# Kernel optimization log

Measured on AMD Instinct MI355X. Metric: run time of the kernel, lower is better.

## Reference

```python
import jax, jax.numpy as jnp
import numpy as np

DIM = 256
HEADS = 8
DIM_HEAD = 64
INNER = HEADS * DIM_HEAD  # 512
SCALE = DIM_HEAD ** -0.5
EPS = 1e-5


def _layernorm(x, w, b):
    mu = jnp.mean(x, axis=-1, keepdims=True)
    var = jnp.var(x, axis=-1, keepdims=True)
    return (x - mu) * jax.lax.rsqrt(var + EPS) * w + b


def setup_inputs() -> dict:
    key = jax.random.key(0)
    ks = jax.random.split(key, 20)
    B, N, M, H, W = 8, 4096, 256, 64, 64
    s = 0.02
    inp = {
        "feat": jax.random.normal(ks[0], (B, N, DIM), jnp.float32),
        "center": jax.random.normal(ks[1], (B, M, DIM), jnp.float32),
        "pos": jax.random.normal(ks[2], (B, DIM, H, W), jnp.float32),
        "center_pos": jax.random.normal(ks[3], (B, M, DIM), jnp.float32),
        # projection weights stored [in, out] so y = x @ W
        "Wq": jax.random.normal(ks[4], (DIM, INNER), jnp.float32) * s,
        "Wk": jax.random.normal(ks[5], (DIM, INNER), jnp.float32) * s,
        "Wv1": jax.random.normal(ks[6], (DIM, INNER), jnp.float32) * s,
        "Wv2": jax.random.normal(ks[7], (DIM, INNER), jnp.float32) * s,
        "Wo1": jax.random.normal(ks[8], (INNER, DIM), jnp.float32) * s,
        "Wo2": jax.random.normal(ks[9], (INNER, DIM), jnp.float32) * s,
        "ln1_w": jnp.ones((DIM,), jnp.float32),
        "ln1_b": jnp.zeros((DIM,), jnp.float32),
        "ln2_w": jnp.ones((DIM,), jnp.float32),
        "ln2_b": jnp.zeros((DIM,), jnp.float32),
        "ffn1_W1": jax.random.normal(ks[10], (DIM, DIM), jnp.float32) * s,
        "ffn1_W2": jax.random.normal(ks[11], (DIM, DIM), jnp.float32) * s,
        "ffn1_b2": jnp.zeros((DIM,), jnp.float32),
        "ffn2_W1": jax.random.normal(ks[12], (DIM, DIM), jnp.float32) * s,
        "ffn2_W2": jax.random.normal(ks[13], (DIM, DIM), jnp.float32) * s,
        "ffn2_b2": jnp.zeros((DIM,), jnp.float32),
    }
    return inp


def reference(feat, center, pos, center_pos, Wq, Wk, Wv1, Wv2, Wo1, Wo2,
              ln1_w, ln1_b, ln2_w, ln2_b, ffn1_W1, ffn1_W2, ffn1_b2,
              ffn2_W1, ffn2_W2, ffn2_b2):
    B = feat.shape[0]
    # pos: [B, C, H, W] -> [B, N, C]
    pos_f = pos.reshape(B, DIM, -1).transpose(0, 2, 1)
    q = (feat + pos_f) @ Wq            # [B, N, INNER]
    k = (center + center_pos) @ Wk     # [B, M, INNER]
    v1 = feat @ Wv1                    # [B, N, INNER]
    v2 = center @ Wv2                  # [B, M, INNER]

    def split(x):  # [B, T, h*d] -> [B, h, T, d]
        return x.reshape(B, x.shape[1], HEADS, DIM_HEAD).transpose(0, 2, 1, 3)

    q, k, v1, v2 = split(q), split(k), split(v1), split(v2)
    attn = jnp.einsum("bhnd,bhmd->bhnm", q, k) * SCALE  # [B, h, N, M]
    attn1 = jax.nn.softmax(attn, axis=-2)  # over N (queries)
    attn2 = jax.nn.softmax(attn, axis=-1)  # over M (keys)
    out_feat = jnp.einsum("bhnm,bhmd->bhnd", attn2, v2)    # [B, h, N, d]
    out_center = jnp.einsum("bhnm,bhnd->bhmd", attn1, v1)  # [B, h, M, d]

    def merge(x):  # [B, h, T, d] -> [B, T, h*d]
        return x.transpose(0, 2, 1, 3).reshape(B, x.shape[2], INNER)

    out_feat = merge(out_feat) @ Wo1 + feat
    out_center = merge(out_center) @ Wo2 + center
    out_feat = _layernorm(out_feat, ln1_w, ln1_b)
    out_center = _layernorm(out_center, ln2_w, ln2_b)
    out_feat = jax.nn.relu(out_feat @ ffn1_W1) @ ffn1_W2 + ffn1_b2 + out_feat
    out_center = jax.nn.relu(out_center @ ffn2_W1) @ ffn2_W2 + ffn2_b2 + out_center
    return out_feat, out_center
```

## Files before the change

### kernel.cpp

```cpp
#include <hip/hip_runtime.h>

typedef __bf16 bf16;
typedef __bf16 bf16x4 __attribute__((ext_vector_type(4)));
typedef __bf16 bf16x8 __attribute__((ext_vector_type(8)));
typedef float f32x4 __attribute__((ext_vector_type(4)));

#define MFMA16(a, b, c) __builtin_amdgcn_mfma_f32_16x16x32_bf16(a, b, c, 0, 0, 0)

#define CEXP 0.18033688011112042f

struct WTArgs {
  const float* src[10];
  bf16* dst[10];
  int K[10];
  int N[10];
};

__global__ __launch_bounds__(256) void wtrans_kernel(WTArgs args) {
  const int z = blockIdx.z;
  const int K = args.K[z], N = args.N[z];
  const int k0 = blockIdx.x * 64, n0 = blockIdx.y * 64;
  if (k0 >= K || n0 >= N) return;
  __shared__ float t[64][65];
  const int tx = threadIdx.x & 63, ty = threadIdx.x >> 6;
  const float* __restrict__ src = args.src[z];
  bf16* __restrict__ dst = args.dst[z];
#pragma unroll
  for (int i = 0; i < 16; ++i)
    t[ty + i * 4][tx] = src[(size_t)(k0 + ty + i * 4) * N + n0 + tx];
  __syncthreads();
#pragma unroll
  for (int i = 0; i < 16; ++i)
    dst[(size_t)(n0 + ty + i * 4) * K + k0 + tx] = (bf16)t[tx][ty + i * 4];
}

__global__ __launch_bounds__(256) void prep_xq_kernel(
    const float* __restrict__ feat, const float* __restrict__ pos,
    bf16* __restrict__ xq) {
  const int n0 = blockIdx.x * 64;
  const int c0 = blockIdx.y * 64;
  const int b = blockIdx.z;
  __shared__ float t[64][65];
  const int tx = threadIdx.x & 63, ty = threadIdx.x >> 6;
#pragma unroll
  for (int i = 0; i < 16; ++i) {
    int c = ty + i * 4;
    t[c][tx] = pos[((size_t)b * 256 + c0 + c) * 4096 + n0 + tx];
  }
  __syncthreads();
#pragma unroll
  for (int i = 0; i < 16; ++i) {
    int n = ty + i * 4;
    size_t off = ((size_t)b * 4096 + n0 + n) * 256 + c0 + tx;
    xq[off] = (bf16)(feat[off] + t[tx][n]);
  }
}

__global__ __launch_bounds__(256) void addvec_kernel(
    const float* __restrict__ a, const float* __restrict__ b,
    bf16* __restrict__ o, int n4) {
  int i = blockIdx.x * 256 + threadIdx.x;
  if (i < n4) {
    f32x4 x = ((const f32x4*)a)[i];
    f32x4 y = ((const f32x4*)b)[i];
    bf16x4 z;
#pragma unroll
    for (int j = 0; j < 4; ++j) z[j] = (bf16)(x[j] + y[j]);
    ((bf16x4*)o)[i] = z;
  }
}

template <typename TA>
__device__ inline bf16x8 ldA8(const TA* p);
template <>
__device__ inline bf16x8 ldA8<bf16>(const bf16* p) {
  return *(const bf16x8*)p;
}
template <>
__device__ inline bf16x8 ldA8<float>(const float* p) {
  f32x4 u = *(const f32x4*)p;
  f32x4 v = *((const f32x4*)p + 1);
  bf16x8 o;
#pragma unroll
  for (int i = 0; i < 4; ++i) {
    o[i] = (bf16)u[i];
    o[4 + i] = (bf16)v[i];
  }
  return o;
}

template <int EPI, typename TO, typename TR, typename TA>
__global__ __launch_bounds__(256) void gemm_kernel(
    const TA* __restrict__ A, const bf16* __restrict__ BT,
    TO* __restrict__ C, const TR* __restrict__ resid,
    const float* __restrict__ bias, int M, int N, int K) {
  const int m0 = blockIdx.x * 128;
  const int n0 = blockIdx.y * 128;
  const int tid = threadIdx.x;
  const int lane = tid & 63;
  const int w = tid >> 6;
  const int wr = (w >> 1) * 64, wc = (w & 1) * 64;
  const int l15 = lane & 15, quad = lane >> 4;

  __shared__ bf16 Al[128 * 40];
  __shared__ bf16 Bl[128 * 40];

  f32x4 acc[4][4];
#pragma unroll
  for (int i = 0; i < 4; ++i)
#pragma unroll
    for (int j = 0; j < 4; ++j) acc[i][j] = (f32x4){0.f, 0.f, 0.f, 0.f};

  for (int k0 = 0; k0 < K; k0 += 32) {
#pragma unroll
    for (int c = 0; c < 2; ++c) {
      int idx = tid + c * 256;
      int row = idx >> 2;
      int ko = (idx & 3) * 8;
      *(bf16x8*)(Al + row * 40 + ko) =
          ldA8(A + (size_t)(m0 + row) * K + k0 + ko);
      *(bf16x8*)(Bl + row * 40 + ko) =
          *(const bf16x8*)(BT + (size_t)(n0 + row) * K + k0 + ko);
    }
    __syncthreads();
    bf16x8 fa[4], fb[4];
#pragma unroll
    for (int i = 0; i < 4; ++i) {
      fa[i] = *(const bf16x8*)(Al + (wr + i * 16 + l15) * 40 + quad * 8);
      fb[i] = *(const bf16x8*)(Bl + (wc + i * 16 + l15) * 40 + quad * 8);
    }
#pragma unroll
    for (int i = 0; i < 4; ++i)
#pragma unroll
      for (int j = 0; j < 4; ++j)
        acc[i][j] = MFMA16(fa[i], fb[j], acc[i][j]);
    __syncthreads();
  }

#pragma unroll
  for (int i = 0; i < 4; ++i) {
#pragma unroll
    for (int r = 0; r < 4; ++r) {
      int row = m0 + wr + i * 16 + quad * 4 + r;
      size_t rb = (size_t)row * N + n0 + wc;
#pragma unroll
      for (int j = 0; j < 4; ++j) {
        int col = j * 16 + l15;
        float v = acc[i][j][r];
        if constexpr (EPI == 1) v = fmaxf(v, 0.f);
        if constexpr (EPI == 2) v += (float)resid[rb + col];
        if constexpr (EPI == 3)
          v += bias[n0 + wc + col] + (float)resid[rb + col];
        C[rb + col] = (TO)v;
      }
    }
  }
}

__global__ __launch_bounds__(256) void attf_kernel(
    const bf16* q, const bf16* __restrict__ kk, const bf16* __restrict__ v1,
    const bf16* __restrict__ v2, bf16* af, float* __restrict__ acc_c,
    float* __restrict__ colsum) {
  const int nb = blockIdx.x;
  const int h = blockIdx.y;
  const int b = blockIdx.z;
  const int tid = threadIdx.x;
  const int lane = tid & 63;
  const int w = tid >> 6;
  const int l15 = lane & 15, quad = lane >> 4;

  __shared__ bf16 klds[64 * 72];
  __shared__ bf16 v2T[64 * 72];
  __shared__ bf16 v1T[64 * 72];
  __shared__ bf16 PT[64 * 72];
  __shared__ bf16 Pl[4][16 * 72];

  f32x4 oc2[16];
#pragma unroll
  for (int i = 0; i < 16; ++i) oc2[i] = (f32x4){0.f, 0.f, 0.f, 0.f};
  float cs[16];
#pragma unroll
  for (int i = 0; i < 16; ++i) cs[i] = 0.f;

  for (int ch = 0; ch < 8; ++ch) {
    int nrow = b * 4096 + nb * 512 + ch * 64 + w * 16 + l15;
    const bf16* qp = q + (size_t)nrow * 512 + h * 64 + quad * 8;
    bf16x8 a0 = *(const bf16x8*)(qp);
    bf16x8 a1 = *(const bf16x8*)(qp + 32);

    f32x4 o1[4];
#pragma unroll
    for (int i = 0; i < 4; ++i) o1[i] = (f32x4){0.f, 0.f, 0.f, 0.f};
    float rs[4] = {0.f, 0.f, 0.f, 0.f};

    for (int mq = 0; mq < 4; ++mq) {
      __syncthreads();
#pragma unroll
      for (int c = 0; c < 2; ++c) {
        int idx = tid + c * 256;
        int m = idx >> 3, dc = (idx & 7) * 8;
        *(bf16x8*)(klds + m * 72 + dc) = *(const bf16x8*)(
            kk + ((size_t)(b * 256 + mq * 64 + m)) * 512 + h * 64 + dc);
      }
#pragma unroll
      for (int c = 0; c < 16; ++c) {
        int idx = tid + c * 256;
        int m = idx >> 6, d = idx & 63;
        v2T[d * 72 + m] =
            v2[((size_t)(b * 256 + mq * 64 + m)) * 512 + h * 64 + d];
      }
      if (mq == 0) {
#pragma unroll
        for (int c = 0; c < 16; ++c) {
          int idx = tid + c * 256;
          int nl = idx >> 6, d = idx & 63;
          v1T[d * 72 + nl] = v1[((size_t)(b * 4096 + nb * 512 + ch * 64 + nl)) *
                                    512 + h * 64 + d];
        }
      }
      __syncthreads();

#pragma unroll
      for (int mt = 0; mt < 4; ++mt) {
        const bf16* kp = klds + (mt * 16 + l15) * 72 + quad * 8;
        bf16x8 b0 = *(const bf16x8*)(kp);
        bf16x8 b1 = *(const bf16x8*)(kp + 32);
        f32x4 s = (f32x4){0.f, 0.f, 0.f, 0.f};
        s = MFMA16(a0, b0, s);
        s = MFMA16(a1, b1, s);
        float e0 = exp2f(s[0] * CEXP);
        float e1 = exp2f(s[1] * CEXP);
        float e2 = exp2f(s[2] * CEXP);
        float e3 = exp2f(s[3] * CEXP);
        rs[0] += e0; rs[1] += e1; rs[2] += e2; rs[3] += e3;
        cs[mq * 4 + mt] += e0 + e1 + e2 + e3;
        Pl[w][(quad * 4 + 0) * 72 + mt * 16 + l15] = (bf16)e0;
        Pl[w][(quad * 4 + 1) * 72 + mt * 16 + l15] = (bf16)e1;
        Pl[w][(quad * 4 + 2) * 72 + mt * 16 + l15] = (bf16)e2;
        Pl[w][(quad * 4 + 3) * 72 + mt * 16 + l15] = (bf16)e3;
        bf16x4 ev;
        ev[0] = (bf16)e0; ev[1] = (bf16)e1; ev[2] = (bf16)e2; ev[3] = (bf16)e3;
        *(bf16x4*)(PT + (mt * 16 + l15) * 72 + w * 16 + quad * 4) = ev;
      }
      __syncthreads();

#pragma unroll
      for (int ks = 0; ks < 2; ++ks) {
        bf16x8 pa = *(const bf16x8*)(Pl[w] + l15 * 72 + ks * 32 + quad * 8);
#pragma unroll
        for (int dt = 0; dt < 4; ++dt) {
          bf16x8 vb =
              *(const bf16x8*)(v2T + (dt * 16 + l15) * 72 + ks * 32 + quad * 8);
          o1[dt] = MFMA16(pa, vb, o1[dt]);
        }
      }
#pragma unroll
      for (int ks = 0; ks < 2; ++ks) {
        bf16x8 pa2 =
            *(const bf16x8*)(PT + (w * 16 + l15) * 72 + ks * 32 + quad * 8);
#pragma unroll
        for (int dt = 0; dt < 4; ++dt) {
          bf16x8 vb =
              *(const bf16x8*)(v1T + (dt * 16 + l15) * 72 + ks * 32 + quad * 8);
          oc2[mq * 4 + dt] = MFMA16(pa2, vb, oc2[mq * 4 + dt]);
        }
      }
    }

    float inv[4];
#pragma unroll
    for (int r = 0; r < 4; ++r) {
      float v = rs[r];
      v += __shfl_xor(v, 1, 64);
      v += __shfl_xor(v, 2, 64);
      v += __shfl_xor(v, 4, 64);
      v += __shfl_xor(v, 8, 64);
      inv[r] = 1.f / v;
    }
#pragma unroll
    for (int dt = 0; dt < 4; ++dt) {
#pragma unroll
      for (int r = 0; r < 4; ++r) {
        int n = nb * 512 + ch * 64 + w * 16 + quad * 4 + r;
        af[((size_t)(b * 4096 + n)) * 512 + h * 64 + dt * 16 + l15] =
            (bf16)(o1[dt][r] * inv[r]);
      }
    }
  }

#pragma unroll
  for (int t = 0; t < 16; ++t) {
    float v = cs[t];
    v += __shfl_xor(v, 16, 64);
    v += __shfl_xor(v, 32, 64);
    if (quad == 0)
      atomicAdd(&colsum[(b * 8 + h) * 256 + (t >> 2) * 64 + (t & 3) * 16 + l15],
                v);
  }
  float* base = acc_c + ((size_t)(b * 8 + h)) * 256 * 64;
#pragma unroll
  for (int mq = 0; mq < 4; ++mq) {
#pragma unroll
    for (int dt = 0; dt < 4; ++dt) {
#pragma unroll
      for (int r = 0; r < 4; ++r) {
        int m = mq * 64 + w * 16 + quad * 4 + r;
        atomicAdd(base + m * 64 + dt * 16 + l15, oc2[mq * 4 + dt][r]);
      }
    }
  }
}

__global__ __launch_bounds__(256) void acm_kernel(
    const float* __restrict__ acc_c, const float* __restrict__ colsum,
    bf16* __restrict__ acm) {
  int idx = blockIdx.x * 256 + threadIdx.x;
  int d = idx & 63;
  int h = (idx >> 6) & 7;
  int m = (idx >> 9) & 255;
  int b = idx >> 17;
  float cv = colsum[(b * 8 + h) * 256 + m];
  float v = acc_c[(((size_t)(b * 8 + h)) * 256 + m) * 64 + d] / cv;
  acm[idx] = (bf16)v;
}

__global__ __launch_bounds__(256) void ln_kernel(
    const bf16* __restrict__ x, const float* __restrict__ wv,
    const float* __restrict__ bv, bf16* __restrict__ y, int rows) {
  int wave = threadIdx.x >> 6;
  int lane = threadIdx.x & 63;
  int row = blockIdx.x * 4 + wave;
  if (row >= rows) return;
  const bf16* xr = x + (size_t)row * 256;
  bf16x4 v = *(const bf16x4*)(xr + lane * 4);
  float f0 = v[0], f1 = v[1], f2 = v[2], f3 = v[3];
  float s = f0 + f1 + f2 + f3;
  float ss = f0 * f0 + f1 * f1 + f2 * f2 + f3 * f3;
#pragma unroll
  for (int m = 1; m < 64; m <<= 1) {
    s += __shfl_xor(s, m, 64);
    ss += __shfl_xor(ss, m, 64);
  }
  float mean = s * (1.f / 256.f);
  float var = ss * (1.f / 256.f) - mean * mean;
  float rstd = rsqrtf(var + 1e-5f);
  f32x4 wq = *(const f32x4*)(wv + lane * 4);
  f32x4 bq = *(const f32x4*)(bv + lane * 4);
  bf16x4 o;
  o[0] = (bf16)((f0 - mean) * rstd * wq[0] + bq[0]);
  o[1] = (bf16)((f1 - mean) * rstd * wq[1] + bq[1]);
  o[2] = (bf16)((f2 - mean) * rstd * wq[2] + bq[2]);
  o[3] = (bf16)((f3 - mean) * rstd * wq[3] + bq[3]);
  *(bf16x4*)(y + (size_t)row * 256 + lane * 4) = o;
}

extern "C" void kernel_launch(void* const* d_in, const int* in_sizes, int n_in,
                              void* d_out, int out_size, void* d_ws,
                              size_t ws_size, hipStream_t stream) {
  const float* feat = (const float*)d_in[0];
  const float* center = (const float*)d_in[1];
  const float* pos = (const float*)d_in[2];
  const float* cpos = (const float*)d_in[3];
  const float* Wq = (const float*)d_in[4];
  const float* Wk = (const float*)d_in[5];
  const float* Wv1 = (const float*)d_in[6];
  const float* Wv2 = (const float*)d_in[7];
  const float* Wo1 = (const float*)d_in[8];
  const float* Wo2 = (const float*)d_in[9];
  const float* ln1w = (const float*)d_in[10];
  const float* ln1b = (const float*)d_in[11];
  const float* ln2w = (const float*)d_in[12];
  const float* ln2b = (const float*)d_in[13];
  const float* f1W1 = (const float*)d_in[14];
  const float* f1W2 = (const float*)d_in[15];
  const float* f1b2 = (const float*)d_in[16];
  const float* f2W1 = (const float*)d_in[17];
  const float* f2W2 = (const float*)d_in[18];
  const float* f2b2 = (const float*)d_in[19];

  char* ws = (char*)d_ws;
  const size_t MB = 1024 * 1024;
  bf16* q_ = (bf16*)(ws + 0);
  bf16* af_ = q_;
  bf16* v1_ = (bf16*)(ws + 32 * MB);
  bf16* xq_ = (bf16*)(ws + 64 * MB);
  bf16* rf_ = xq_;
  bf16* k_ = (bf16*)(ws + 80 * MB);
  bf16* xk_ = (bf16*)(ws + 82 * MB);
  bf16* rc_ = xk_;
  bf16* v2_ = (bf16*)(ws + 83 * MB);
  bf16* acm_ = v2_;
  float* acc_ = (float*)(ws + 85 * MB);
  float* colsum_ = (float*)(ws + 89 * MB);
  bf16* wt_ = (bf16*)(ws + 89 * MB + 65536);
  bf16* yf_ = q_;
  bf16* tf_ = (bf16*)(ws + 16 * MB);
  bf16* yc_ = (bf16*)(ws + 92 * MB);
  bf16* tc_ = (bf16*)(ws + 93 * MB);

  bf16* WqT = wt_;
  bf16* WkT = WqT + 131072;
  bf16* Wv1T = WkT + 131072;
  bf16* Wv2T = Wv1T + 131072;
  bf16* Wo1T = Wv2T + 131072;
  bf16* Wo2T = Wo1T + 131072;
  bf16* f1W1T = Wo2T + 131072;
  bf16* f1W2T = f1W1T + 65536;
  bf16* f2W1T = f1W2T + 65536;
  bf16* f2W2T = f2W1T + 65536;

  float* out_feat = (float*)d_out;
  float* out_center = out_feat + (size_t)8 * 4096 * 256;

  WTArgs wa;
  const float* srcs[10] = {Wq, Wk, Wv1, Wv2, Wo1, Wo2, f1W1, f1W2, f2W1, f2W2};
  bf16* dsts[10] = {WqT, WkT, Wv1T, Wv2T, Wo1T, Wo2T, f1W1T, f1W2T, f2W1T, f2W2T};
  int Ks[10] = {256, 256, 256, 256, 512, 512, 256, 256, 256, 256};
  int Ns[10] = {512, 512, 512, 512, 256, 256, 256, 256, 256, 256};
  for (int i = 0; i < 10; ++i) {
    wa.src[i] = srcs[i];
    wa.dst[i] = dsts[i];
    wa.K[i] = Ks[i];
    wa.N[i] = Ns[i];
  }

  wtrans_kernel<<<dim3(8, 8, 10), 256, 0, stream>>>(wa);
  prep_xq_kernel<<<dim3(64, 4, 8), 256, 0, stream>>>(feat, pos, xq_);
  addvec_kernel<<<dim3(512), 256, 0, stream>>>(center, cpos, xk_, 131072);
  hipMemsetAsync(ws + 85 * MB, 0, 4 * MB + 65536, stream);

  gemm_kernel<0, bf16, bf16, bf16><<<dim3(256, 4), 256, 0, stream>>>(
      xq_, WqT, q_, nullptr, nullptr, 32768, 512, 256);
  gemm_kernel<0, bf16, bf16, bf16><<<dim3(16, 4), 256, 0, stream>>>(
      xk_, WkT, k_, nullptr, nullptr, 2048, 512, 256);
  gemm_kernel<0, bf16, bf16, float><<<dim3(256, 4), 256, 0, stream>>>(
      feat, Wv1T, v1_, nullptr, nullptr, 32768, 512, 256);
  gemm_kernel<0, bf16, bf16, float><<<dim3(16, 4), 256, 0, stream>>>(
      center, Wv2T, v2_, nullptr, nullptr, 2048, 512, 256);

  attf_kernel<<<dim3(8, 8, 8), 256, 0, stream>>>(q_, k_, v1_, v2_, af_, acc_,
                                                 colsum_);
  acm_kernel<<<dim3(4096), 256, 0, stream>>>(acc_, colsum_, acm_);

  gemm_kernel<2, bf16, float, bf16><<<dim3(256, 2), 256, 0, stream>>>(
      af_, Wo1T, rf_, feat, nullptr, 32768, 256, 512);
  ln_kernel<<<dim3(8192), 256, 0, stream>>>(rf_, ln1w, ln1b, yf_, 32768);
  gemm_kernel<1, bf16, bf16, bf16><<<dim3(256, 2), 256, 0, stream>>>(
      yf_, f1W1T, tf_, nullptr, nullptr, 32768, 256, 256);
  gemm_kernel<3, float, bf16, bf16><<<dim3(256, 2), 256, 0, stream>>>(
      tf_, f1W2T, out_feat, yf_, f1b2, 32768, 256, 256);

  gemm_kernel<2, bf16, float, bf16><<<dim3(16, 2), 256, 0, stream>>>(
      acm_, Wo2T, rc_, center, nullptr, 2048, 256, 512);
  ln_kernel<<<dim3(512), 256, 0, stream>>>(rc_, ln2w, ln2b, yc_, 2048);
  gemm_kernel<1, bf16, bf16, bf16><<<dim3(16, 2), 256, 0, stream>>>(
      yc_, f2W1T, tc_, nullptr, nullptr, 2048, 256, 256);
  gemm_kernel<3, float, bf16, bf16><<<dim3(16, 2), 256, 0, stream>>>(
      tc_, f2W2T, out_center, yc_, f2b2, 2048, 256, 256);
}
```

Baseline: 439.7 us.

## Keep all keys resident in LDS and replace attention atomics with partial buffers

The attention kernel now loads all 256 keys and the transposed V2 into LDS once per block instead of reloading them for every 64-row query chunk. Each block now covers 1024 query rows, with 256 blocks instead of 512. The V1 tile for the next chunk is double-buffered and prefetched, and the next Q fragment is loaded while the current PV matmul runs. Global atomics for column sums and center accumulators are replaced by per-block partial buffers, which acm_kernel reduces, so the memset can be dropped. The cost is much larger LDS use (one block per CU via launch_bounds) and fewer blocks, which may reduce occupancy and latency hiding.

```diff
diff --git a/kernel.cpp b/kernel.cpp
--- a/kernel.cpp
+++ b/kernel.cpp
@@ -157,10 +157,10 @@
   }
 }
 
-__global__ __launch_bounds__(256) void attf_kernel(
+__global__ __launch_bounds__(256, 1) void attf_kernel(
     const bf16* q, const bf16* __restrict__ kk, const bf16* __restrict__ v1,
-    const bf16* __restrict__ v2, bf16* af, float* __restrict__ acc_c,
-    float* __restrict__ colsum) {
+    const bf16* __restrict__ v2, bf16* af, float* __restrict__ acc_p,
+    float* __restrict__ colsum_p) {
   const int nb = blockIdx.x;
   const int h = blockIdx.y;
   const int b = blockIdx.z;
@@ -169,11 +169,50 @@
   const int w = tid >> 6;
   const int l15 = lane & 15, quad = lane >> 4;
 
-  __shared__ bf16 klds[64 * 72];
-  __shared__ bf16 v2T[64 * 72];
-  __shared__ bf16 v1T[64 * 72];
-  __shared__ bf16 PT[64 * 72];
-  __shared__ bf16 Pl[4][16 * 72];
+  __shared__ __align__(16) bf16 klds[256 * 72];
+  __shared__ __align__(16) bf16 v2T[64 * 264];
+  __shared__ __align__(16) bf16 v1T[2][64 * 72];
+  __shared__ __align__(16) bf16 PT[256 * 72];
+  __shared__ __align__(16) bf16 Pl[4][16 * 264];
+
+#pragma unroll
+  for (int c = 0; c < 8; ++c) {
+    int idx = tid + c * 256;
+    int m = idx >> 3;
+    int dc = (idx & 7) * 8;
+    *(bf16x8*)(klds + m * 72 + dc) =
+        *(const bf16x8*)(kk + ((size_t)(b * 256 + m)) * 512 + h * 64 + dc);
+  }
+#pragma unroll
+  for (int c = 0; c < 8; ++c) {
+    int idx = tid + c * 256;
+    int m = idx >> 3;
+    int dc = (idx & 7) * 8;
+    bf16x8 t =
+        *(const bf16x8*)(v2 + ((size_t)(b * 256 + m)) * 512 + h * 64 + dc);
+#pragma unroll
+    for (int j = 0; j < 8; ++j) v2T[(dc + j) * 264 + m] = t[j];
+  }
+  {
+    const int nl = tid >> 3;
+    const int dc = (tid & 7) * 8;
+    const bf16* v1b =
+        v1 + ((size_t)(b * 4096 + nb * 1024)) * 512 + h * 64 + dc;
+    bf16x8 t0 = *(const bf16x8*)(v1b + (size_t)nl * 512);
+    bf16x8 t1 = *(const bf16x8*)(v1b + (size_t)(nl + 32) * 512);
+#pragma unroll
+    for (int j = 0; j < 8; ++j) {
+      v1T[0][(dc + j) * 72 + nl] = t0[j];
+      v1T[0][(dc + j) * 72 + nl + 32] = t1[j];
+    }
+  }
+  bf16x8 qa0, qa1;
+  {
+    int nrow = b * 4096 + nb * 1024 + w * 16 + l15;
+    const bf16* qp = q + (size_t)nrow * 512 + h * 64 + quad * 8;
+    qa0 = *(const bf16x8*)(qp);
+    qa1 = *(const bf16x8*)(qp + 32);
+  }
 
   f32x4 oc2[16];
 #pragma unroll
@@ -182,91 +221,74 @@
 #pragma unroll
   for (int i = 0; i < 16; ++i) cs[i] = 0.f;
 
-  for (int ch = 0; ch < 8; ++ch) {
-    int nrow = b * 4096 + nb * 512 + ch * 64 + w * 16 + l15;
-    const bf16* qp = q + (size_t)nrow * 512 + h * 64 + quad * 8;
-    bf16x8 a0 = *(const bf16x8*)(qp);
-    bf16x8 a1 = *(const bf16x8*)(qp + 32);
+  __syncthreads();
+
+#pragma unroll 2
+  for (int ch = 0; ch < 16; ++ch) {
+    bf16x8 v1ra, v1rb;
+    const int nl = tid >> 3;
+    const int dc = (tid & 7) * 8;
+    if (ch < 15) {
+      const bf16* v1b =
+          v1 + ((size_t)(b * 4096 + nb * 1024 + (ch + 1) * 64)) * 512 +
+          h * 64 + dc;
+      v1ra = *(const bf16x8*)(v1b + (size_t)nl * 512);
+      v1rb = *(const bf16x8*)(v1b + (size_t)(nl + 32) * 512);
+    }
+
+    float rs[4] = {0.f, 0.f, 0.f, 0.f};
+#pragma unroll
+    for (int mt = 0; mt < 16; ++mt) {
+      const bf16* kp = klds + (mt * 16 + l15) * 72 + quad * 8;
+      bf16x8 b0 = *(const bf16x8*)(kp);
+      bf16x8 b1 = *(const bf16x8*)(kp + 32);
+      f32x4 s = (f32x4){0.f, 0.f, 0.f, 0.f};
+      s = MFMA16(qa0, b0, s);
+      s = MFMA16(qa1, b1, s);
+      float e0 = exp2f(s[0] * CEXP);
+      float e1 = exp2f(s[1] * CEXP);
+      float e2 = exp2f(s[2] * CEXP);
+      float e3 = exp2f(s[3] * CEXP);
+      rs[0] += e0; rs[1] += e1; rs[2] += e2; rs[3] += e3;
+      cs[mt] += e0 + e1 + e2 + e3;
+      Pl[w][(quad * 4 + 0) * 264 + mt * 16 + l15] = (bf16)e0;
+      Pl[w][(quad * 4 + 1) * 264 + mt * 16 + l15] = (bf16)e1;
+      Pl[w][(quad * 4 + 2) * 264 + mt * 16 + l15] = (bf16)e2;
+      Pl[w][(quad * 4 + 3) * 264 + mt * 16 + l15] = (bf16)e3;
+      bf16x4 ev;
+      ev[0] = (bf16)e0; ev[1] = (bf16)e1; ev[2] = (bf16)e2; ev[3] = (bf16)e3;
+      *(bf16x4*)(PT + (mt * 16 + l15) * 72 + w * 16 + quad * 4) = ev;
+    }
+    if (ch < 15) {
+      bf16* dst = v1T[(ch + 1) & 1];
+#pragma unroll
+      for (int j = 0; j < 8; ++j) {
+        dst[(dc + j) * 72 + nl] = v1ra[j];
+        dst[(dc + j) * 72 + nl + 32] = v1rb[j];
+      }
+    }
+    __syncthreads();
+
+    if (ch < 15) {
+      int nrow = b * 4096 + nb * 1024 + (ch + 1) * 64 + w * 16 + l15;
+      const bf16* qp = q + (size_t)nrow * 512 + h * 64 + quad * 8;
+      qa0 = *(const bf16x8*)(qp);
+      qa1 = *(const bf16x8*)(qp + 32);
+    }
 
     f32x4 o1[4];
 #pragma unroll
     for (int i = 0; i < 4; ++i) o1[i] = (f32x4){0.f, 0.f, 0.f, 0.f};
-    float rs[4] = {0.f, 0.f, 0.f, 0.f};
-
-    for (int mq = 0; mq < 4; ++mq) {
-      __syncthreads();
-#pragma unroll
-      for (int c = 0; c < 2; ++c) {
-        int idx = tid + c * 256;
-        int m = idx >> 3, dc = (idx & 7) * 8;
-        *(bf16x8*)(klds + m * 72 + dc) = *(const bf16x8*)(
-            kk + ((size_t)(b * 256 + mq * 64 + m)) * 512 + h * 64 + dc);
+#pragma unroll
+    for (int ks = 0; ks < 8; ++ks) {
+      bf16x8 pa = *(const bf16x8*)(Pl[w] + l15 * 264 + ks * 32 + quad * 8);
+#pragma unroll
+      for (int dt = 0; dt < 4; ++dt) {
+        bf16x8 vb = *(const bf16x8*)(v2T + (dt * 16 + l15) * 264 + ks * 32 +
+                                     quad * 8);
+        o1[dt] = MFMA16(pa, vb, o1[dt]);
       }
-#pragma unroll
-      for (int c = 0; c < 16; ++c) {
-        int idx = tid + c * 256;
-        int m = idx >> 6, d = idx & 63;
-        v2T[d * 72 + m] =
-            v2[((size_t)(b * 256 + mq * 64 + m)) * 512 + h * 64 + d];
-      }
-      if (mq == 0) {
-#pragma unroll
-        for (int c = 0; c < 16; ++c) {
-          int idx = tid + c * 256;
-          int nl = idx >> 6, d = idx & 63;
-          v1T[d * 72 + nl] = v1[((size_t)(b * 4096 + nb * 512 + ch * 64 + nl)) *
-                                    512 + h * 64 + d];
-        }
-      }
-      __syncthreads();
-
-#pragma unroll
-      for (int mt = 0; mt < 4; ++mt) {
-        const bf16* kp = klds + (mt * 16 + l15) * 72 + quad * 8;
-        bf16x8 b0 = *(const bf16x8*)(kp);
-        bf16x8 b1 = *(const bf16x8*)(kp + 32);
-        f32x4 s = (f32x4){0.f, 0.f, 0.f, 0.f};
-        s = MFMA16(a0, b0, s);
-        s = MFMA16(a1, b1, s);
-        float e0 = exp2f(s[0] * CEXP);
-        float e1 = exp2f(s[1] * CEXP);
-        float e2 = exp2f(s[2] * CEXP);
-        float e3 = exp2f(s[3] * CEXP);
-        rs[0] += e0; rs[1] += e1; rs[2] += e2; rs[3] += e3;
-        cs[mq * 4 + mt] += e0 + e1 + e2 + e3;
-        Pl[w][(quad * 4 + 0) * 72 + mt * 16 + l15] = (bf16)e0;
-        Pl[w][(quad * 4 + 1) * 72 + mt * 16 + l15] = (bf16)e1;
-        Pl[w][(quad * 4 + 2) * 72 + mt * 16 + l15] = (bf16)e2;
-        Pl[w][(quad * 4 + 3) * 72 + mt * 16 + l15] = (bf16)e3;
-        bf16x4 ev;
-        ev[0] = (bf16)e0; ev[1] = (bf16)e1; ev[2] = (bf16)e2; ev[3] = (bf16)e3;
-        *(bf16x4*)(PT + (mt * 16 + l15) * 72 + w * 16 + quad * 4) = ev;
-      }
-      __syncthreads();
-
-#pragma unroll
-      for (int ks = 0; ks < 2; ++ks) {
-        bf16x8 pa = *(const bf16x8*)(Pl[w] + l15 * 72 + ks * 32 + quad * 8);
-#pragma unroll
-        for (int dt = 0; dt < 4; ++dt) {
-          bf16x8 vb =
-              *(const bf16x8*)(v2T + (dt * 16 + l15) * 72 + ks * 32 + quad * 8);
-          o1[dt] = MFMA16(pa, vb, o1[dt]);
-        }
-      }
-#pragma unroll
-      for (int ks = 0; ks < 2; ++ks) {
-        bf16x8 pa2 =
-            *(const bf16x8*)(PT + (w * 16 + l15) * 72 + ks * 32 + quad * 8);
-#pragma unroll
-        for (int dt = 0; dt < 4; ++dt) {
-          bf16x8 vb =
-              *(const bf16x8*)(v1T + (dt * 16 + l15) * 72 + ks * 32 + quad * 8);
-          oc2[mq * 4 + dt] = MFMA16(pa2, vb, oc2[mq * 4 + dt]);
-        }
-      }
-    }
-
+    }
     float inv[4];
 #pragma unroll
     for (int r = 0; r < 4; ++r) {
@@ -281,23 +303,47 @@
     for (int dt = 0; dt < 4; ++dt) {
 #pragma unroll
       for (int r = 0; r < 4; ++r) {
-        int n = nb * 512 + ch * 64 + w * 16 + quad * 4 + r;
+        int n = nb * 1024 + ch * 64 + w * 16 + quad * 4 + r;
         af[((size_t)(b * 4096 + n)) * 512 + h * 64 + dt * 16 + l15] =
             (bf16)(o1[dt][r] * inv[r]);
       }
     }
-  }
-
+
+    const bf16* v1cur = v1T[ch & 1];
+#pragma unroll
+    for (int ks = 0; ks < 2; ++ks) {
+      bf16x8 vb[4];
+#pragma unroll
+      for (int dt = 0; dt < 4; ++dt)
+        vb[dt] = *(const bf16x8*)(v1cur + (dt * 16 + l15) * 72 + ks * 32 +
+                                  quad * 8);
+#pragma unroll
+      for (int mq = 0; mq < 4; ++mq) {
+        bf16x8 pa2 = *(const bf16x8*)(PT + (mq * 64 + w * 16 + l15) * 72 +
+                                      ks * 32 + quad * 8);
+#pragma unroll
+        for (int dt = 0; dt < 4; ++dt)
+          oc2[mq * 4 + dt] = MFMA16(pa2, vb[dt], oc2[mq * 4 + dt]);
+      }
+    }
+    __syncthreads();
+  }
+
+  float* cw = (float*)klds;
 #pragma unroll
   for (int t = 0; t < 16; ++t) {
     float v = cs[t];
     v += __shfl_xor(v, 16, 64);
     v += __shfl_xor(v, 32, 64);
-    if (quad == 0)
-      atomicAdd(&colsum[(b * 8 + h) * 256 + (t >> 2) * 64 + (t & 3) * 16 + l15],
-                v);
-  }
-  float* base = acc_c + ((size_t)(b * 8 + h)) * 256 * 64;
+    if (quad == 0) cw[w * 256 + t * 16 + l15] = v;
+  }
+  __syncthreads();
+  {
+    int m = tid;
+    float s = cw[m] + cw[256 + m] + cw[512 + m] + cw[768 + m];
+    colsum_p[((size_t)(nb * 64 + b * 8 + h)) * 256 + m] = s;
+  }
+  float* base = acc_p + ((size_t)(nb * 64 + b * 8 + h)) * 256 * 64;
 #pragma unroll
   for (int mq = 0; mq < 4; ++mq) {
 #pragma unroll
@@ -305,23 +351,27 @@
 #pragma unroll
       for (int r = 0; r < 4; ++r) {
         int m = mq * 64 + w * 16 + quad * 4 + r;
-        atomicAdd(base + m * 64 + dt * 16 + l15, oc2[mq * 4 + dt][r]);
+        base[m * 64 + dt * 16 + l15] = oc2[mq * 4 + dt][r];
       }
     }
   }
 }
 
 __global__ __launch_bounds__(256) void acm_kernel(
-    const float* __restrict__ acc_c, const float* __restrict__ colsum,
+    const float* __restrict__ acc_p, const float* __restrict__ colsum_p,
     bf16* __restrict__ acm) {
   int idx = blockIdx.x * 256 + threadIdx.x;
   int d = idx & 63;
   int h = (idx >> 6) & 7;
   int m = (idx >> 9) & 255;
   int b = idx >> 17;
-  float cv = colsum[(b * 8 + h) * 256 + m];
-  float v = acc_c[(((size_t)(b * 8 + h)) * 256 + m) * 64 + d] / cv;
-  acm[idx] = (bf16)v;
+  float cv = 0.f, v = 0.f;
+#pragma unroll
+  for (int p = 0; p < 4; ++p) {
+    cv += colsum_p[((size_t)(p * 64 + b * 8 + h)) * 256 + m];
+    v += acc_p[(((size_t)(p * 64 + b * 8 + h)) * 256 + m) * 64 + d];
+  }
+  acm[idx] = (bf16)(v / cv);
 }
 
 __global__ __launch_bounds__(256) void ln_kernel(
@@ -384,15 +434,15 @@
   bf16* af_ = q_;
   bf16* v1_ = (bf16*)(ws + 32 * MB);
   bf16* xq_ = (bf16*)(ws + 64 * MB);
+  float* accp_ = (float*)(ws + 64 * MB);
   bf16* rf_ = xq_;
   bf16* k_ = (bf16*)(ws + 80 * MB);
   bf16* xk_ = (bf16*)(ws + 82 * MB);
   bf16* rc_ = xk_;
   bf16* v2_ = (bf16*)(ws + 83 * MB);
   bf16* acm_ = v2_;
-  float* acc_ = (float*)(ws + 85 * MB);
   float* colsum_ = (float*)(ws + 89 * MB);
-  bf16* wt_ = (bf16*)(ws + 89 * MB + 65536);
+  bf16* wt_ = (bf16*)(ws + 89 * MB + 262144);
   bf16* yf_ = q_;
   bf16* tf_ = (bf16*)(ws + 16 * MB);
   bf16* yc_ = (bf16*)(ws + 92 * MB);
@@ -427,7 +477,6 @@
   wtrans_kernel<<<dim3(8, 8, 10), 256, 0, stream>>>(wa);
   prep_xq_kernel<<<dim3(64, 4, 8), 256, 0, stream>>>(feat, pos, xq_);
   addvec_kernel<<<dim3(512), 256, 0, stream>>>(center, cpos, xk_, 131072);
-  hipMemsetAsync(ws + 85 * MB, 0, 4 * MB + 65536, stream);
 
   gemm_kernel<0, bf16, bf16, bf16><<<dim3(256, 4), 256, 0, stream>>>(
       xq_, WqT, q_, nullptr, nullptr, 32768, 512, 256);
@@ -438,9 +487,9 @@
   gemm_kernel<0, bf16, bf16, float><<<dim3(16, 4), 256, 0, stream>>>(
       center, Wv2T, v2_, nullptr, nullptr, 2048, 512, 256);
 
-  attf_kernel<<<dim3(8, 8, 8), 256, 0, stream>>>(q_, k_, v1_, v2_, af_, acc_,
+  attf_kernel<<<dim3(4, 8, 8), 256, 0, stream>>>(q_, k_, v1_, v2_, af_, accp_,
                                                  colsum_);
-  acm_kernel<<<dim3(4096), 256, 0, stream>>>(acc_, colsum_, acm_);
+  acm_kernel<<<dim3(4096), 256, 0, stream>>>(accp_, colsum_, acm_);
 
   gemm_kernel<2, bf16, float, bf16><<<dim3(256, 2), 256, 0, stream>>>(
       af_, Wo1T, rf_, feat, nullptr, 32768, 256, 512);
```

Result: faster. 391.5 us (-11.0%).
